# Kernel tuning notes

Hardware: AMD Instinct MI355X
Metric: run time of the kernel (lower is better)

Reference implementation:

```python
import jax, jax.numpy as jnp
import numpy as np

N_NODES = 40000
N_EDGES = 640000
N_GRAPHS = 64
F_IN = 32       # fourier_order*4
D_EMB = 256     # int(0.5*512)
D_HID = 512     # int(0.5*1024)
D_FC = 1024     # int(0.5*2048)
N_CLS = 10


def setup_inputs() -> dict:
    key = jax.random.key(0)
    ks = iter(jax.random.split(key, 40))
    rn = lambda shape, s=0.05: jax.random.normal(next(ks), shape, jnp.float32) * s
    inp = {
        'x': jax.random.normal(next(ks), (N_NODES, F_IN), jnp.float32),
        'edge_index': jax.random.randint(next(ks), (2, N_EDGES), 0, N_NODES, jnp.int32),
        'edge_attr': jax.random.uniform(next(ks), (N_EDGES, 1), jnp.float32),
        'batch': jnp.sort(jax.random.randint(next(ks), (N_NODES,), 0, N_GRAPHS, jnp.int32)),
        # embedding MLP
        'emb_w1': rn((F_IN, D_EMB)), 'emb_b1': jnp.zeros((D_EMB,), jnp.float32),
        'emb_w2': rn((D_EMB, D_EMB)), 'emb_b2': jnp.zeros((D_EMB,), jnp.float32),
        # edge_proj MLP
        'ep_w1': rn((1, 64)), 'ep_b1': jnp.zeros((64,), jnp.float32),
        'ep_w2': rn((64, 1)), 'ep_b2': jnp.zeros((1,), jnp.float32),
        # GCNConv weights (x @ W + b, PyG convention)
        'w_c1': rn((D_EMB, D_HID)), 'b_c1': jnp.zeros((D_HID,), jnp.float32),
        'w_c2': rn((D_HID, D_HID)), 'b_c2': jnp.zeros((D_HID,), jnp.float32),
        'w_c3': rn((D_HID, D_HID)), 'b_c3': jnp.zeros((D_HID,), jnp.float32),
        'w_c4': rn((D_HID, D_HID)), 'b_c4': jnp.zeros((D_HID,), jnp.float32),
        'w_c5': rn((D_HID, D_HID)), 'b_c5': jnp.zeros((D_HID,), jnp.float32),
        'w_c6': rn((D_HID, D_HID)), 'b_c6': jnp.zeros((D_HID,), jnp.float32),
        # head
        'fc1_w': rn((D_HID, D_FC)), 'fc1_b': jnp.zeros((D_FC,), jnp.float32),
        'head_w': rn((D_FC, N_CLS)), 'head_b': jnp.zeros((N_CLS,), jnp.float32),
    }
    return inp


def _gcn_conv(x, src, dst, norm, W, b):
    # PyG GCNConv: linear transform, then normalized scatter-add aggregation, then bias
    h = x @ W                                   # [N, d_out]
    msg = h[src] * norm[:, None]                # [E+N, d_out] gathered messages
    agg = jax.ops.segment_sum(msg, dst, num_segments=N_NODES)
    return agg + b


def _forward(x, edge_attr, emb_w1, emb_b1, emb_w2, emb_b2, ep_w1, ep_b1, ep_w2, ep_b2,
             w_c1, b_c1, w_c2, b_c2, w_c3, b_c3, w_c4, b_c4, w_c5, b_c5, w_c6, b_c6,
             fc1_w, fc1_b, head_w, head_b, edge_index, batch):
    # edge weights from edge_proj MLP (sigmoid output in (0,1))
    ew = jax.nn.sigmoid(jax.nn.relu(edge_attr @ ep_w1 + ep_b1) @ ep_w2 + ep_b2)[:, 0]  # [E]
    # gcn_norm with self loops (identical for every conv layer -> compute once)
    loops = jnp.arange(N_NODES, dtype=edge_index.dtype)
    src = jnp.concatenate([edge_index[0], loops])
    dst = jnp.concatenate([edge_index[1], loops])
    w = jnp.concatenate([ew, jnp.ones((N_NODES,), ew.dtype)])
    deg = jax.ops.segment_sum(w, dst, num_segments=N_NODES)
    dinv = jnp.where(deg > 0, jax.lax.rsqrt(jnp.maximum(deg, 1e-12)), 0.0)
    norm = dinv[src] * w * dinv[dst]            # [E+N]

    h = jax.nn.relu(jax.nn.relu(x @ emb_w1 + emb_b1) @ emb_w2 + emb_b2)
    h = _gcn_conv(h, src, dst, norm, w_c1, b_c1)
    skip = jax.nn.relu(h)
    h = _gcn_conv(skip, src, dst, norm, w_c2, b_c2)
    h = jax.nn.relu(h)
    h = _gcn_conv(h, src, dst, norm, w_c3, b_c3)
    skip = jax.nn.relu(h) + skip                # has_skip=True
    h = _gcn_conv(skip, src, dst, norm, w_c4, b_c4)  # is_deep=True
    h = jax.nn.relu(h)
    h = _gcn_conv(h, src, dst, norm, w_c5, b_c5)
    h = jax.nn.relu(h)
    h = _gcn_conv(h, src, dst, norm, w_c6, b_c6)
    skip = jax.nn.relu(h) + skip

    # global mean pool over graphs
    sums = jax.ops.segment_sum(skip, batch, num_segments=N_GRAPHS)
    cnts = jax.ops.segment_sum(jnp.ones((N_NODES,), skip.dtype), batch, num_segments=N_GRAPHS)
    pooled = sums / jnp.maximum(cnts, 1.0)[:, None]   # [G, D_HID]

    out = jax.nn.relu(pooled @ fc1_w + fc1_b) @ head_w + head_b   # [G, N_CLS]
    return out


def reference(x, edge_index, edge_attr, batch, emb_w1, emb_b1, emb_w2, emb_b2,
              ep_w1, ep_b1, ep_w2, ep_b2, w_c1, b_c1, w_c2, b_c2, w_c3, b_c3,
              w_c4, b_c4, w_c5, b_c5, w_c6, b_c6, fc1_w, fc1_b, head_w, head_b):
    return _forward(x, edge_attr, emb_w1, emb_b1, emb_w2, emb_b2, ep_w1, ep_b1, ep_w2, ep_b2,
                    w_c1, b_c1, w_c2, b_c2, w_c3, b_c3, w_c4, b_c4, w_c5, b_c5, w_c6, b_c6,
                    fc1_w, fc1_b, head_w, head_b, edge_index, batch)
```

## Files before the change

kernel.cpp:

```cpp
#include <hip/hip_runtime.h>
#include <math.h>

#define N_NODES 40000
#define MP      40192
#define NROWB   157
#define N_EDGES 640000
#define N_GRAPHS 64
#define F_IN 32
#define D_EMB 256
#define D_HID 512
#define D_FC 1024
#define N_CLS 10

typedef _Float16 f16x8 __attribute__((ext_vector_type(8)));
typedef float f32x4  __attribute__((ext_vector_type(4)));
typedef unsigned short u16;

template <int N> struct VecU;
template <> struct VecU<2> { typedef unsigned T __attribute__((ext_vector_type(2))); };
template <> struct VecU<4> { typedef unsigned T __attribute__((ext_vector_type(4))); };

__device__ __forceinline__ float h2f(u16 u) {
    union { u16 s; _Float16 h; } v; v.s = u; return (float)v.h;
}
__device__ __forceinline__ u16 f2h(float f) {
    union { u16 s; _Float16 h; } v; v.h = (_Float16)f; return v.s;
}
__device__ __forceinline__ void async16(void* lds, const void* g) {
    __builtin_amdgcn_global_load_lds((const __attribute__((address_space(1))) void*)g,
                                     (__attribute__((address_space(3))) void*)lds, 16, 0, 0);
}
__device__ __forceinline__ void fma_mix2(float& a0, float& a1, unsigned u, float v) {
    asm("v_fma_mix_f32 %0, %2, %3, %0 op_sel:[0,0,0] op_sel_hi:[1,0,0]\n\t"
        "v_fma_mix_f32 %1, %2, %3, %1 op_sel:[1,0,0] op_sel_hi:[1,0,0]"
        : "+v"(a0), "+v"(a1) : "v"(u), "v"(v));
}

__device__ __forceinline__ int pk_idx(int r, int q) {
    int rp = r >> 1;
    int g  = (((r & 1) << 2) | q) ^ (rp & 7);
    return rp * 64 + g * 8;
}

__global__ void prep_all(const float* __restrict__ x, u16* __restrict__ xb, u16* __restrict__ G,
                         float* __restrict__ deg, int* __restrict__ cnt, int* __restrict__ cursor,
                         float* __restrict__ sums) {
    int i = blockIdx.x * blockDim.x + threadIdx.x;
    if (i < N_NODES) { deg[i] = 1.0f; cnt[i] = 0; cursor[i] = 0; }
    if (i < MP * F_IN) {
        int row = i >> 5, colk = i & 31;
        float v = (row < N_NODES) ? x[i] : 0.f;
        size_t idx = (size_t)(row >> 8) * 8192 + pk_idx(row & 255, colk >> 3) + (colk & 7);
        xb[idx] = f2h(v);
    }
    if (i < 16 * 3072) {
        int kc = i / 3072, rem = i % 3072;
        G[(size_t)(156 * 16 + kc) * 8192 + 5120 + rem] = 0;
    } else if (i < 16 * 3072 + 8 * 3072) {
        int j = i - 16 * 3072;
        int kc = j / 3072, rem = j % 3072;
        G[(size_t)(156 * 8 + kc) * 8192 + 5120 + rem] = 0;
    }
    if (i < N_GRAPHS * D_HID) sums[i] = 0.f;
}

__global__ void edge_mlp_deg(const float* __restrict__ edge_attr,
                             const float* __restrict__ ep_w1, const float* __restrict__ ep_b1,
                             const float* __restrict__ ep_w2, const float* __restrict__ ep_b2,
                             const int* __restrict__ dst,
                             float* __restrict__ ew, float* __restrict__ deg, int* __restrict__ cnt) {
    __shared__ float w1[64], b1[64], w2[64];
    int t = threadIdx.x;
    if (t < 64) { w1[t] = ep_w1[t]; b1[t] = ep_b1[t]; w2[t] = ep_w2[t]; }
    __syncthreads();
    int e = blockIdx.x * blockDim.x + t;
    if (e >= N_EDGES) return;
    float x = edge_attr[e];
    float s = ep_b2[0];
#pragma unroll
    for (int j = 0; j < 64; ++j) s += fmaxf(x * w1[j] + b1[j], 0.f) * w2[j];
    float sig = 1.f / (1.f + expf(-s));
    ew[e] = sig;
    int d = dst[e];
    atomicAdd(&deg[d], sig);
    atomicAdd(&cnt[d], 1);
}

__global__ void dinv_kernel(const float* __restrict__ deg, float* __restrict__ dinv,
                            float* __restrict__ nloop) {
    int i = blockIdx.x * blockDim.x + threadIdx.x;
    if (i >= N_NODES) return;
    float d = deg[i];
    float r = (d > 0.f) ? rsqrtf(fmaxf(d, 1e-12f)) : 0.f;
    dinv[i] = r;
    nloop[i] = r * r;
}

__global__ void scan_kernel(const int* __restrict__ cnt, int* __restrict__ rowptr) {
    __shared__ int part[1024];
    int t = threadIdx.x;
    const int PER = (N_NODES + 1023) / 1024;
    int base = t * PER;
    int s = 0;
    for (int k = 0; k < PER; ++k) { int i = base + k; if (i < N_NODES) s += cnt[i]; }
    part[t] = s;
    __syncthreads();
    for (int off = 1; off < 1024; off <<= 1) {
        int v = (t >= off) ? part[t - off] : 0;
        __syncthreads();
        part[t] += v;
        __syncthreads();
    }
    int run = (t == 0) ? 0 : part[t - 1];
    for (int k = 0; k < PER; ++k) {
        int i = base + k;
        if (i < N_NODES) { rowptr[i] = run; run += cnt[i]; }
    }
    if (t == 1023) rowptr[N_NODES] = run;
}

__global__ void fill_csr_kernel(const int* __restrict__ src, const int* __restrict__ dst,
                                const float* __restrict__ ew, const float* __restrict__ dinv,
                                const int* __restrict__ rowptr, int* __restrict__ cursor,
                                int2* __restrict__ cv) {
    int e = blockIdx.x * blockDim.x + threadIdx.x;
    if (e >= N_EDGES) return;
    int d = dst[e];
    int s = src[e];
    float n = dinv[s] * ew[e] * dinv[d];
    int p = rowptr[d] + atomicAdd(&cursor[d], 1);
    cv[p] = make_int2(s, __float_as_int(n));
}

struct WPair { const float* s; u16* d; int K; int N; };
struct WP8 { WPair m[8]; };

__global__ void wprep_all(WP8 a) {
    __shared__ u16 th[32][33];
    WPair w = a.m[blockIdx.z];
    int n0 = blockIdx.x * 32;
    int k0 = blockIdx.y * 32;
    if (n0 >= w.N || k0 >= w.K) return;
    int tx = threadIdx.x, ty = threadIdx.y;
#pragma unroll
    for (int r = 0; r < 4; ++r) {
        int k = ty + r * 8;
        th[k][tx] = f2h(w.s[(size_t)(k0 + k) * w.N + n0 + tx]);
    }
    __syncthreads();
#pragma unroll
    for (int r = 0; r < 4; ++r) {
        int n = ty + r * 8;
        int R = n0 + n;
        int kcol = k0 + tx;
        size_t idx = ((size_t)(R >> 7) * (w.K >> 5) + (kcol >> 5)) * 4096
                   + pk_idx(R & 127, (kcol >> 3) & 3) + (kcol & 7);
        w.d[idx] = th[tx][n];
    }
}

__launch_bounds__(512)
__global__ void mfma_gemm(const u16* __restrict__ A,
                          const u16* __restrict__ W,
                          const float* __restrict__ bias,
                          const u16* __restrict__ skip,
                          u16* __restrict__ C, u16* __restrict__ Cpk,
                          int K, int N,
                          const int* __restrict__ batch, float* __restrict__ pool) {
    __shared__ __align__(16) u16 Wl[32768];
    __shared__ int sbatch[128];

    const int nColB = N >> 6;
    int b = blockIdx.x;
    int rowI = (b >> 3) / nColB * 8 + (b & 7);
    int colI = (b >> 3) % nColB;
    if (rowI >= NROWB) return;
    int rowBase = rowI * 256;
    int colBase = colI * 64;

    int t = threadIdx.x;
    int lane = t & 63;
    int wave = t >> 6;
    int quad = lane >> 4;
    int mrow = lane & 15;
    int nIter = K >> 5;

    int sw = (((mrow & 1) << 2) | quad) ^ ((mrow >> 1) & 7);
    int laneA = (wave * 16 + (mrow >> 1)) * 64 + sw * 8;
    int laneW = (mrow >> 1) * 64 + sw * 8;

    const u16* pA = A + (size_t)rowI * nIter * 8192;

    f16x8 aA0 = *(const f16x8*)&pA[laneA];
    f16x8 aA1 = *(const f16x8*)&pA[laneA + 512];
    f16x8 aB0, aB1;

    {
        const u16* ws = W + ((size_t)(colI >> 1) * nIter) * 4096 + (colI & 1) * 2048;
        for (int kc = wave; kc < nIter; kc += 8) {
            const u16* s = ws + (size_t)kc * 4096;
            u16* d = &Wl[kc * 2048];
            async16(&d[0],    s + lane * 8);
            async16(&d[512],  s + 512 + lane * 8);
            async16(&d[1024], s + 1024 + lane * 8);
            async16(&d[1536], s + 1536 + lane * 8);
        }
    }
    asm volatile("s_waitcnt vmcnt(0)" ::: "memory");
    __syncthreads();

    f32x4 acc[2][4] = {};

    for (int it = 0; it < nIter; it += 2) {
        if (it + 1 < nIter) {
            const u16* nA = pA + (size_t)(it + 1) * 8192;
            aB0 = *(const f16x8*)&nA[laneA];
            aB1 = *(const f16x8*)&nA[laneA + 512];
        }
        __builtin_amdgcn_sched_barrier(0);
        {
            const u16* Wc = &Wl[it * 2048];
#pragma unroll
            for (int j = 0; j < 4; ++j) {
                f16x8 w = *(const f16x8*)&Wc[laneW + j * 512];
                acc[0][j] = __builtin_amdgcn_mfma_f32_16x16x32_f16(aA0, w, acc[0][j], 0, 0, 0);
                acc[1][j] = __builtin_amdgcn_mfma_f32_16x16x32_f16(aA1, w, acc[1][j], 0, 0, 0);
            }
        }
        if (it + 1 < nIter) {
            if (it + 2 < nIter) {
                const u16* nA = pA + (size_t)(it + 2) * 8192;
                aA0 = *(const f16x8*)&nA[laneA];
                aA1 = *(const f16x8*)&nA[laneA + 512];
            }
            __builtin_amdgcn_sched_barrier(0);
            const u16* Wc = &Wl[(it + 1) * 2048];
#pragma unroll
            for (int j = 0; j < 4; ++j) {
                f16x8 w = *(const f16x8*)&Wc[laneW + j * 512];
                acc[0][j] = __builtin_amdgcn_mfma_f32_16x16x32_f16(aB0, w, acc[0][j], 0, 0, 0);
                acc[1][j] = __builtin_amdgcn_mfma_f32_16x16x32_f16(aB1, w, acc[1][j], 0, 0, 0);
            }
        }
    }
    __syncthreads();

    u16* eb = Wl;
    const int ES = 72;
#pragma unroll
    for (int ph = 0; ph < 2; ++ph) {
        if ((wave >> 2) == ph) {
#pragma unroll
            for (int j = 0; j < 4; ++j) {
                int col = colBase + j * 16 + mrow;
                float bv = bias[col];
#pragma unroll
                for (int i = 0; i < 2; ++i) {
#pragma unroll
                    for (int r = 0; r < 4; ++r) {
                        int lr = (wave & 3) * 32 + i * 16 + quad * 4 + r;
                        size_t row = (size_t)rowBase + ph * 128 + lr;
                        float v = fmaxf(acc[i][j][r] + bv, 0.f);
                        if (skip) v += h2f(skip[row * N + col]);
                        eb[lr * ES + j * 16 + mrow] = f2h(v);
                    }
                }
            }
        }
        if (pool && t < 128) {
            int row = rowBase + ph * 128 + t;
            sbatch[t] = (row < N_NODES) ? batch[row] : -1;
        }
        __syncthreads();
        if (C) {
#pragma unroll
            for (int k2 = 0; k2 < 2; ++k2) {
                int c = t + k2 * 512;
                int row = c >> 3, ch = c & 7;
                f16x8 v = *(const f16x8*)&eb[row * ES + ch * 8];
                *(f16x8*)&C[(size_t)(rowBase + ph * 128 + row) * N + colBase + ch * 8] = v;
            }
        } else if (Cpk) {
#pragma unroll
            for (int k2 = 0; k2 < 2; ++k2) {
                int c = t + k2 * 512;
                int row = c >> 3, ch = c & 7;
                f16x8 v = *(const f16x8*)&eb[row * ES + ch * 8];
                size_t idx = ((size_t)rowI * (N >> 5) + (colBase >> 5) + (ch >> 2)) * 8192
                           + pk_idx(ph * 128 + row, ch & 3);
                *(f16x8*)&Cpk[idx] = v;
            }
        }
        if (pool) {
            int c = t & 63;
            int rs = (t >> 6) * 16;
            float run = 0.f; int g = -1;
            for (int r = rs; r < rs + 16; ++r) {
                int bg = sbatch[r];
                if (bg != g) {
                    if (g >= 0) atomicAdd(&pool[(size_t)g * D_HID + colBase + c], run);
                    run = 0.f; g = bg;
                }
                if (bg >= 0) run += h2f(eb[r * ES + c]);
            }
            if (g >= 0) atomicAdd(&pool[(size_t)g * D_HID + colBase + c], run);
        }
        __syncthreads();
    }
}

template <int D>
__launch_bounds__(256)
__global__ void gather_f16(const u16* __restrict__ h, const int* __restrict__ rowptr,
                           const int2* __restrict__ cv, const float* __restrict__ nloop,
                           u16* __restrict__ out) {
    constexpr int COLS = D / 8;
    constexpr int LPG  = COLS / 8;
    constexpr int NPB  = 256 / LPG;
    using VU = typename VecU<4>::T;
    int b = blockIdx.x;
    int slice = b & 7;
    int ng = b >> 3;
    int t = threadIdx.x;
    int node = ng * NPB + t / LPG;
    int l = t % LPG;
    if (node >= N_NODES) return;
    const u16* hs = h + slice * COLS + l * 8;
    float acc[8];
    float sl = nloop[node];
    {
        VU own = *(const VU*)(hs + (size_t)node * D);
#pragma unroll
        for (int u = 0; u < 4; ++u) {
            acc[2 * u] = 0.f; acc[2 * u + 1] = 0.f;
            fma_mix2(acc[2 * u], acc[2 * u + 1], own[u], sl);
        }
    }
    int beg = rowptr[node], end = rowptr[node + 1];
    if (end > beg) {
        int last = end - 1;
        int2 c[8];
#pragma unroll
        for (int m = 0; m < 8; ++m) c[m] = cv[min(beg + m, last)];
        for (int j = beg; j < end; j += 8) {
            VU tv[8];
#pragma unroll
            for (int m = 0; m < 8; ++m)
                tv[m] = *(const VU*)(hs + (size_t)c[m].x * D);
            int jn = j + 8;
            int2 cn[8];
#pragma unroll
            for (int m = 0; m < 8; ++m) cn[m] = c[m];
            if (jn < end) {
#pragma unroll
                for (int m = 0; m < 8; ++m) cn[m] = cv[min(jn + m, last)];
            }
            __builtin_amdgcn_sched_barrier(0);
#pragma unroll
            for (int m = 0; m < 8; ++m) {
                float v = (j + m < end) ? __int_as_float(c[m].y) : 0.f;
#pragma unroll
                for (int u = 0; u < 4; ++u)
                    fma_mix2(acc[2 * u], acc[2 * u + 1], tv[m][u], v);
            }
#pragma unroll
            for (int m = 0; m < 8; ++m) c[m] = cn[m];
        }
    }
    VU o;
#pragma unroll
    for (int u = 0; u < 4; ++u) {
        unsigned lo = f2h(acc[2 * u]);
        unsigned hi = f2h(acc[2 * u + 1]);
        o[u] = lo | (hi << 16);
    }
    size_t blkb = (size_t)(node >> 8) * (D >> 5);
    int rr = node & 255;
    int kc, q;
    if (D == 512) { kc = slice * 2 + (l >> 2); q = l & 3; }
    else          { kc = slice;                q = l;     }
    *(VU*)(out + (blkb + kc) * 8192 + pk_idx(rr, q)) = o;
}

__launch_bounds__(1024)
__global__ void fc1_head(const float* __restrict__ sums, const int* __restrict__ batch,
                         const float* __restrict__ fc1_w, const float* __restrict__ fc1_b,
                         const float* __restrict__ head_w, const float* __restrict__ head_b,
                         float* __restrict__ out) {
    __shared__ float sv[D_HID];
    __shared__ float hacc[N_CLS];
    __shared__ float invc;
    int g = blockIdx.x;
    int t = threadIdx.x;
    if (t == 0) {
        int lo = 0, hi = N_NODES;
        while (lo < hi) { int m = (lo + hi) >> 1; if (batch[m] < g) lo = m + 1; else hi = m; }
        int lb = lo;
        lo = lb; hi = N_NODES;
        while (lo < hi) { int m = (lo + hi) >> 1; if (batch[m] < g + 1) lo = m + 1; else hi = m; }
        invc = 1.f / fmaxf((float)(lo - lb), 1.f);
    }
    if (t < N_CLS) hacc[t] = 0.f;
    __syncthreads();
    if (t < D_HID) sv[t] = sums[(size_t)g * D_HID + t] * invc;
    __syncthreads();
    int j = t;
    float acc = fc1_b[j];
#pragma unroll 8
    for (int k = 0; k < D_HID; ++k) acc += sv[k] * fc1_w[(size_t)k * D_FC + j];
    float f = fmaxf(acc, 0.f);
    float p[N_CLS];
#pragma unroll
    for (int c = 0; c < N_CLS; ++c) p[c] = f * head_w[j * N_CLS + c];
#pragma unroll
    for (int c = 0; c < N_CLS; ++c) {
        float v = p[c];
        for (int off = 32; off; off >>= 1) v += __shfl_down(v, off, 64);
        if ((t & 63) == 0) atomicAdd(&hacc[c], v);
    }
    __syncthreads();
    if (t < N_CLS) out[g * N_CLS + t] = hacc[t] + head_b[t];
}

extern "C" void kernel_launch(void* const* d_in, const int* in_sizes, int n_in,
                              void* d_out, int out_size, void* d_ws, size_t ws_size,
                              hipStream_t stream) {
    const float* x          = (const float*)d_in[0];
    const int*   edge_index = (const int*)d_in[1];
    const float* edge_attr  = (const float*)d_in[2];
    const int*   batch      = (const int*)d_in[3];
    const float* emb_w1 = (const float*)d_in[4];
    const float* emb_b1 = (const float*)d_in[5];
    const float* emb_w2 = (const float*)d_in[6];
    const float* emb_b2 = (const float*)d_in[7];
    const float* ep_w1  = (const float*)d_in[8];
    const float* ep_b1  = (const float*)d_in[9];
    const float* ep_w2  = (const float*)d_in[10];
    const float* ep_b2  = (const float*)d_in[11];
    const float* w_c[6] = { (const float*)d_in[12], (const float*)d_in[14], (const float*)d_in[16],
                            (const float*)d_in[18], (const float*)d_in[20], (const float*)d_in[22] };
    const float* b_c[6] = { (const float*)d_in[13], (const float*)d_in[15], (const float*)d_in[17],
                            (const float*)d_in[19], (const float*)d_in[21], (const float*)d_in[23] };
    const float* fc1_w  = (const float*)d_in[24];
    const float* fc1_b  = (const float*)d_in[25];
    const float* head_w = (const float*)d_in[26];
    const float* head_b = (const float*)d_in[27];
    float* out = (float*)d_out;

    const int* src = edge_index;
    const int* dst = edge_index + N_EDGES;

    char* p = (char*)d_ws;
    auto alloc = [&](size_t bytes) { char* r = p; p += (bytes + 255) & ~(size_t)255; return r; };
    float* ew    = (float*)alloc(N_EDGES * 4);
    float* deg   = (float*)alloc(N_NODES * 4);
    float* dinv  = (float*)alloc(N_NODES * 4);
    float* nloop = (float*)alloc(N_NODES * 4);
    int* cnt     = (int*)alloc(N_NODES * 4);
    int* cursor  = (int*)alloc(N_NODES * 4);
    int* rowptr  = (int*)alloc((N_NODES + 1) * 4);
    int2* cv     = (int2*)alloc((size_t)N_EDGES * 8);
    u16* xb = (u16*)alloc((size_t)MP * F_IN * 2);
    u16* H1 = (u16*)alloc((size_t)MP * D_EMB * 2);
    u16* H2 = (u16*)alloc((size_t)MP * D_EMB * 2);
    u16* G  = (u16*)alloc((size_t)MP * D_HID * 2);
    u16* S1 = (u16*)alloc((size_t)MP * D_HID * 2);
    u16* S2 = (u16*)alloc((size_t)MP * D_HID * 2);
    u16* Cb = (u16*)alloc((size_t)MP * D_HID * 2);
    u16* we1 = (u16*)alloc((size_t)F_IN * D_EMB * 2);
    u16* we2 = (u16*)alloc((size_t)D_EMB * D_EMB * 2);
    u16* wc[6];
    wc[0] = (u16*)alloc((size_t)D_EMB * D_HID * 2);
    for (int i = 1; i < 6; ++i) wc[i] = (u16*)alloc((size_t)D_HID * D_HID * 2);
    float* sums = (float*)alloc(N_GRAPHS * D_HID * 4);

    const int TB = 256;
    const int EB = (N_EDGES + TB - 1) / TB;
    const int NB = (N_NODES + TB - 1) / TB;

    prep_all<<<(MP * F_IN + TB - 1) / TB, TB, 0, stream>>>(x, xb, G, deg, cnt, cursor, sums);
    edge_mlp_deg<<<EB, TB, 0, stream>>>(edge_attr, ep_w1, ep_b1, ep_w2, ep_b2, dst, ew, deg, cnt);
    dinv_kernel<<<NB, TB, 0, stream>>>(deg, dinv, nloop);
    scan_kernel<<<1, 1024, 0, stream>>>(cnt, rowptr);
    fill_csr_kernel<<<EB, TB, 0, stream>>>(src, dst, ew, dinv, rowptr, cursor, cv);

    WP8 wp;
    wp.m[0] = { emb_w1, we1, F_IN,  D_EMB };
    wp.m[1] = { emb_w2, we2, D_EMB, D_EMB };
    wp.m[2] = { w_c[0], wc[0], D_EMB, D_HID };
    for (int i = 1; i < 6; ++i) wp.m[2 + i] = { w_c[i], wc[i], D_HID, D_HID };
    wprep_all<<<dim3(16, 16, 8), dim3(32, 8), 0, stream>>>(wp);

    const int SLOTS = ((NROWB + 7) / 8) * 8;
    const int GRID2 = SLOTS * (D_EMB / 64);
    const int GRID4 = SLOTS * (D_HID / 64);
    mfma_gemm<<<GRID2, 512, 0, stream>>>(xb, we1, emb_b1, nullptr, nullptr, H1, F_IN, D_EMB, nullptr, nullptr);
    mfma_gemm<<<GRID2, 512, 0, stream>>>(H1, we2, emb_b2, nullptr, H2, nullptr, D_EMB, D_EMB, nullptr, nullptr);

    const int GG256 = (N_NODES / 64) * 8;
    const int GG512 = (N_NODES / 32) * 8;
    gather_f16<D_EMB><<<GG256, 256, 0, stream>>>(H2, rowptr, cv, nloop, G);
    mfma_gemm<<<GRID4, 512, 0, stream>>>(G, wc[0], b_c[0], nullptr, S1, nullptr, D_EMB, D_HID, nullptr, nullptr);
    gather_f16<D_HID><<<GG512, 256, 0, stream>>>(S1, rowptr, cv, nloop, G);
    mfma_gemm<<<GRID4, 512, 0, stream>>>(G, wc[1], b_c[1], nullptr, Cb, nullptr, D_HID, D_HID, nullptr, nullptr);
    gather_f16<D_HID><<<GG512, 256, 0, stream>>>(Cb, rowptr, cv, nloop, G);
    mfma_gemm<<<GRID4, 512, 0, stream>>>(G, wc[2], b_c[2], S1, S2, nullptr, D_HID, D_HID, nullptr, nullptr);
    gather_f16<D_HID><<<GG512, 256, 0, stream>>>(S2, rowptr, cv, nloop, G);
    mfma_gemm<<<GRID4, 512, 0, stream>>>(G, wc[3], b_c[3], nullptr, Cb, nullptr, D_HID, D_HID, nullptr, nullptr);
    gather_f16<D_HID><<<GG512, 256, 0, stream>>>(Cb, rowptr, cv, nloop, G);
    mfma_gemm<<<GRID4, 512, 0, stream>>>(G, wc[4], b_c[4], nullptr, Cb, nullptr, D_HID, D_HID, nullptr, nullptr);
    gather_f16<D_HID><<<GG512, 256, 0, stream>>>(Cb, rowptr, cv, nloop, G);
    mfma_gemm<<<GRID4, 512, 0, stream>>>(G, wc[5], b_c[5], S2, nullptr, nullptr, D_HID, D_HID, batch, sums);

    fc1_head<<<N_GRAPHS, 1024, 0, stream>>>(sums, batch, fc1_w, fc1_b, head_w, head_b, out);
}
```

Before: 1.061 ms.

## Stream GEMM weights from global into registers instead of staging all of W in LDS

The GEMM kernel no longer async-copies the whole weight panel (up to 64KB) into LDS before the K loop. Each wave now loads its weight fragments straight from global memory into registers, double-buffered alongside the A fragments. The epilogue writes all 256 output rows in a single pass through a smaller LDS buffer, so one barrier replaces the previous two-phase loop. This removes the up-front LDS fill and its barrier and cuts LDS use, which may allow more blocks per CU. In exchange every wave re-reads W from global or L2, and more registers are held live for the prefetched fragments.

After: 1.034 ms. -2.5%, faster.

```diff
diff --git a/kernel.cpp b/kernel.cpp
--- a/kernel.cpp
+++ b/kernel.cpp
@@ -25,10 +25,6 @@
 }
 __device__ __forceinline__ u16 f2h(float f) {
     union { u16 s; _Float16 h; } v; v.h = (_Float16)f; return v.s;
-}
-__device__ __forceinline__ void async16(void* lds, const void* g) {
-    __builtin_amdgcn_global_load_lds((const __attribute__((address_space(1))) void*)g,
-                                     (__attribute__((address_space(3))) void*)lds, 16, 0, 0);
 }
 __device__ __forceinline__ void fma_mix2(float& a0, float& a1, unsigned u, float v) {
     asm("v_fma_mix_f32 %0, %2, %3, %0 op_sel:[0,0,0] op_sel_hi:[1,0,0]\n\t"
@@ -167,8 +163,8 @@
                           u16* __restrict__ C, u16* __restrict__ Cpk,
                           int K, int N,
                           const int* __restrict__ batch, float* __restrict__ pool) {
-    __shared__ __align__(16) u16 Wl[32768];
-    __shared__ int sbatch[128];
+    __shared__ __align__(16) u16 eb[256 * 72];
+    __shared__ int sbatch[256];
 
     const int nColB = N >> 6;
     int b = blockIdx.x;
@@ -190,122 +186,95 @@
     int laneW = (mrow >> 1) * 64 + sw * 8;
 
     const u16* pA = A + (size_t)rowI * nIter * 8192;
-
-    f16x8 aA0 = *(const f16x8*)&pA[laneA];
-    f16x8 aA1 = *(const f16x8*)&pA[laneA + 512];
-    f16x8 aB0, aB1;
-
-    {
-        const u16* ws = W + ((size_t)(colI >> 1) * nIter) * 4096 + (colI & 1) * 2048;
-        for (int kc = wave; kc < nIter; kc += 8) {
-            const u16* s = ws + (size_t)kc * 4096;
-            u16* d = &Wl[kc * 2048];
-            async16(&d[0],    s + lane * 8);
-            async16(&d[512],  s + 512 + lane * 8);
-            async16(&d[1024], s + 1024 + lane * 8);
-            async16(&d[1536], s + 1536 + lane * 8);
-        }
-    }
-    asm volatile("s_waitcnt vmcnt(0)" ::: "memory");
-    __syncthreads();
+    const u16* pW = W + ((size_t)(colI >> 1) * nIter) * 4096 + (colI & 1) * 2048;
+
+    f16x8 a0 = *(const f16x8*)&pA[laneA];
+    f16x8 a1 = *(const f16x8*)&pA[laneA + 512];
+    f16x8 w0 = *(const f16x8*)&pW[laneW];
+    f16x8 w1 = *(const f16x8*)&pW[laneW + 512];
+    f16x8 w2 = *(const f16x8*)&pW[laneW + 1024];
+    f16x8 w3 = *(const f16x8*)&pW[laneW + 1536];
+    f16x8 na0, na1, nw0, nw1, nw2, nw3;
 
     f32x4 acc[2][4] = {};
 
-    for (int it = 0; it < nIter; it += 2) {
+    for (int it = 0; it < nIter; ++it) {
         if (it + 1 < nIter) {
             const u16* nA = pA + (size_t)(it + 1) * 8192;
-            aB0 = *(const f16x8*)&nA[laneA];
-            aB1 = *(const f16x8*)&nA[laneA + 512];
+            const u16* nW = pW + (size_t)(it + 1) * 4096;
+            na0 = *(const f16x8*)&nA[laneA];
+            na1 = *(const f16x8*)&nA[laneA + 512];
+            nw0 = *(const f16x8*)&nW[laneW];
+            nw1 = *(const f16x8*)&nW[laneW + 512];
+            nw2 = *(const f16x8*)&nW[laneW + 1024];
+            nw3 = *(const f16x8*)&nW[laneW + 1536];
         }
         __builtin_amdgcn_sched_barrier(0);
-        {
-            const u16* Wc = &Wl[it * 2048];
-#pragma unroll
-            for (int j = 0; j < 4; ++j) {
-                f16x8 w = *(const f16x8*)&Wc[laneW + j * 512];
-                acc[0][j] = __builtin_amdgcn_mfma_f32_16x16x32_f16(aA0, w, acc[0][j], 0, 0, 0);
-                acc[1][j] = __builtin_amdgcn_mfma_f32_16x16x32_f16(aA1, w, acc[1][j], 0, 0, 0);
+        acc[0][0] = __builtin_amdgcn_mfma_f32_16x16x32_f16(a0, w0, acc[0][0], 0, 0, 0);
+        acc[1][0] = __builtin_amdgcn_mfma_f32_16x16x32_f16(a1, w0, acc[1][0], 0, 0, 0);
+        acc[0][1] = __builtin_amdgcn_mfma_f32_16x16x32_f16(a0, w1, acc[0][1], 0, 0, 0);
+        acc[1][1] = __builtin_amdgcn_mfma_f32_16x16x32_f16(a1, w1, acc[1][1], 0, 0, 0);
+        acc[0][2] = __builtin_amdgcn_mfma_f32_16x16x32_f16(a0, w2, acc[0][2], 0, 0, 0);
+        acc[1][2] = __builtin_amdgcn_mfma_f32_16x16x32_f16(a1, w2, acc[1][2], 0, 0, 0);
+        acc[0][3] = __builtin_amdgcn_mfma_f32_16x16x32_f16(a0, w3, acc[0][3], 0, 0, 0);
+        acc[1][3] = __builtin_amdgcn_mfma_f32_16x16x32_f16(a1, w3, acc[1][3], 0, 0, 0);
+        a0 = na0; a1 = na1; w0 = nw0; w1 = nw1; w2 = nw2; w3 = nw3;
+    }
+
+    const int ES = 72;
+#pragma unroll
+    for (int j = 0; j < 4; ++j) {
+        int col = colBase + j * 16 + mrow;
+        float bv = bias[col];
+#pragma unroll
+        for (int i = 0; i < 2; ++i) {
+#pragma unroll
+            for (int r = 0; r < 4; ++r) {
+                int lr = (wave >> 2) * 128 + (wave & 3) * 32 + i * 16 + quad * 4 + r;
+                size_t row = (size_t)rowBase + lr;
+                float v = fmaxf(acc[i][j][r] + bv, 0.f);
+                if (skip) v += h2f(skip[row * N + col]);
+                eb[lr * ES + j * 16 + mrow] = f2h(v);
             }
         }
-        if (it + 1 < nIter) {
-            if (it + 2 < nIter) {
-                const u16* nA = pA + (size_t)(it + 2) * 8192;
-                aA0 = *(const f16x8*)&nA[laneA];
-                aA1 = *(const f16x8*)&nA[laneA + 512];
+    }
+    if (pool && t < 256) {
+        int row = rowBase + t;
+        sbatch[t] = (row < N_NODES) ? batch[row] : -1;
+    }
+    __syncthreads();
+    if (C) {
+#pragma unroll
+        for (int k2 = 0; k2 < 4; ++k2) {
+            int c = t + k2 * 512;
+            int row = c >> 3, ch = c & 7;
+            f16x8 v = *(const f16x8*)&eb[row * ES + ch * 8];
+            *(f16x8*)&C[(size_t)(rowBase + row) * N + colBase + ch * 8] = v;
+        }
+    } else if (Cpk) {
+#pragma unroll
+        for (int k2 = 0; k2 < 4; ++k2) {
+            int c = t + k2 * 512;
+            int row = c >> 3, ch = c & 7;
+            f16x8 v = *(const f16x8*)&eb[row * ES + ch * 8];
+            size_t idx = ((size_t)rowI * (N >> 5) + (colBase >> 5) + (ch >> 2)) * 8192
+                       + pk_idx(row, ch & 3);
+            *(f16x8*)&Cpk[idx] = v;
+        }
+    }
+    if (pool) {
+        int c = t & 63;
+        int rs = (t >> 6) * 32;
+        float run = 0.f; int g = -1;
+        for (int r = rs; r < rs + 32; ++r) {
+            int bg = sbatch[r];
+            if (bg != g) {
+                if (g >= 0) atomicAdd(&pool[(size_t)g * D_HID + colBase + c], run);
+                run = 0.f; g = bg;
             }
-            __builtin_amdgcn_sched_barrier(0);
-            const u16* Wc = &Wl[(it + 1) * 2048];
-#pragma unroll
-            for (int j = 0; j < 4; ++j) {
-                f16x8 w = *(const f16x8*)&Wc[laneW + j * 512];
-                acc[0][j] = __builtin_amdgcn_mfma_f32_16x16x32_f16(aB0, w, acc[0][j], 0, 0, 0);
-                acc[1][j] = __builtin_amdgcn_mfma_f32_16x16x32_f16(aB1, w, acc[1][j], 0, 0, 0);
-            }
-        }
-    }
-    __syncthreads();
-
-    u16* eb = Wl;
-    const int ES = 72;
-#pragma unroll
-    for (int ph = 0; ph < 2; ++ph) {
-        if ((wave >> 2) == ph) {
-#pragma unroll
-            for (int j = 0; j < 4; ++j) {
-                int col = colBase + j * 16 + mrow;
-                float bv = bias[col];
-#pragma unroll
-                for (int i = 0; i < 2; ++i) {
-#pragma unroll
-                    for (int r = 0; r < 4; ++r) {
-                        int lr = (wave & 3) * 32 + i * 16 + quad * 4 + r;
-                        size_t row = (size_t)rowBase + ph * 128 + lr;
-                        float v = fmaxf(acc[i][j][r] + bv, 0.f);
-                        if (skip) v += h2f(skip[row * N + col]);
-                        eb[lr * ES + j * 16 + mrow] = f2h(v);
-                    }
-                }
-            }
-        }
-        if (pool && t < 128) {
-            int row = rowBase + ph * 128 + t;
-            sbatch[t] = (row < N_NODES) ? batch[row] : -1;
-        }
-        __syncthreads();
-        if (C) {
-#pragma unroll
-            for (int k2 = 0; k2 < 2; ++k2) {
-                int c = t + k2 * 512;
-                int row = c >> 3, ch = c & 7;
-                f16x8 v = *(const f16x8*)&eb[row * ES + ch * 8];
-                *(f16x8*)&C[(size_t)(rowBase + ph * 128 + row) * N + colBase + ch * 8] = v;
-            }
-        } else if (Cpk) {
-#pragma unroll
-            for (int k2 = 0; k2 < 2; ++k2) {
-                int c = t + k2 * 512;
-                int row = c >> 3, ch = c & 7;
-                f16x8 v = *(const f16x8*)&eb[row * ES + ch * 8];
-                size_t idx = ((size_t)rowI * (N >> 5) + (colBase >> 5) + (ch >> 2)) * 8192
-                           + pk_idx(ph * 128 + row, ch & 3);
-                *(f16x8*)&Cpk[idx] = v;
-            }
-        }
-        if (pool) {
-            int c = t & 63;
-            int rs = (t >> 6) * 16;
-            float run = 0.f; int g = -1;
-            for (int r = rs; r < rs + 16; ++r) {
-                int bg = sbatch[r];
-                if (bg != g) {
-                    if (g >= 0) atomicAdd(&pool[(size_t)g * D_HID + colBase + c], run);
-                    run = 0.f; g = bg;
-                }
-                if (bg >= 0) run += h2f(eb[r * ES + c]);
-            }
-            if (g >= 0) atomicAdd(&pool[(size_t)g * D_HID + colBase + c], run);
-        }
-        __syncthreads();
+            if (bg >= 0) run += h2f(eb[r * ES + c]);
+        }
+        if (g >= 0) atomicAdd(&pool[(size_t)g * D_HID + colBase + c], run);
     }
 }
 
```
